# Performance work log

Hardware: AMD Instinct MI355X
Metric: run time of the kernel (lower is better)

The kernel has to match this reference:

```python
import jax, jax.numpy as jnp
import numpy as np

N = 100000   # nodes
E = 1600000  # edges (avg degree 16)
D = 128      # feature / hidden dim


def setup_inputs() -> dict:
    key = jax.random.key(0)
    k_x, k_e, k_w1, k_w2 = jax.random.split(key, 4)
    scale = 1.0 / np.sqrt(D)
    return {
        "x": jax.random.normal(k_x, (N, D), dtype=jnp.float32),
        "W1": jax.random.normal(k_w1, (D, D), dtype=jnp.float32) * scale,
        "b1": jnp.zeros((D,), dtype=jnp.float32),
        "W2": jax.random.normal(k_w2, (D, D), dtype=jnp.float32) * scale,
        "b2": jnp.zeros((D,), dtype=jnp.float32),
        "edge_index": jax.random.randint(k_e, (2, E), 0, N, dtype=jnp.int64),
    }


def _gcn_conv(h, src, dst, norm, W, b, n_nodes):
    # GCNConv: out = scatter_add(norm * (h @ W)[src] -> dst) + b
    y = h @ W                                   # [N, D] dense GEMM
    msgs = y[src] * norm[:, None]               # [E+N, D] gather + scale
    agg = jax.ops.segment_sum(msgs, dst, num_segments=n_nodes)  # scatter-add
    return agg + b


def reference(x, W1, b1, W2, b2, edge_index):
    n_nodes = x.shape[0]
    # add self loops (GCNConv default add_self_loops=True)
    loop = jnp.arange(n_nodes, dtype=edge_index.dtype)
    src = jnp.concatenate([edge_index[0], loop])
    dst = jnp.concatenate([edge_index[1], loop])
    # symmetric normalization: deg over destinations incl. self loops
    deg = jax.ops.segment_sum(jnp.ones_like(src, dtype=x.dtype), dst,
                              num_segments=n_nodes)
    dinv = jnp.where(deg > 0, jax.lax.rsqrt(deg), 0.0)
    norm = dinv[src] * dinv[dst]                # [E+N]
    # dropout in eval mode (identity); layer = conv -> ReLU, twice
    h = jax.nn.relu(_gcn_conv(x, src, dst, norm, W1, b1, n_nodes))
    h = jax.nn.relu(_gcn_conv(h, src, dst, norm, W2, b2, n_nodes))
    return h
```

## Files before the change

kernel.cpp:

```cpp
#include <hip/hip_runtime.h>
#include <hip/hip_bf16.h>


#define DIM 128
#define BSH 9
#define NBKT 196

typedef __attribute__((ext_vector_type(8))) short bf16x8;
typedef __attribute__((ext_vector_type(4))) float f32x4;

static __device__ __forceinline__ ushort bfbits(float f) {
    __hip_bfloat16 h = __float2bfloat16(f);
    return *(ushort*)&h;
}


__global__ __launch_bounds__(256) void k_bcount(const int* __restrict__ dst,
                                                int E, int* __restrict__ bcnt) {
    __shared__ int h[NBKT];
    int t = threadIdx.x;
    for (int b = t; b < NBKT; b += 256) h[b] = 0;
    __syncthreads();
    for (int e = blockIdx.x * 256 + t; e < E; e += gridDim.x * 256)
        atomicAdd(&h[dst[e] >> BSH], 1);
    __syncthreads();
    for (int b = t; b < NBKT; b += 256)
        if (h[b]) atomicAdd(&bcnt[b], h[b]);
}

__global__ void k_bscan(const int* __restrict__ bcnt, int* __restrict__ bbase,
                        int* __restrict__ bcur) {
    __shared__ int a[256], c[256];
    int t = threadIdx.x;
    int v = (t < NBKT) ? bcnt[t] : 0;
    a[t] = v;
    __syncthreads();
    int* A = a; int* B = c;
    for (int off = 1; off < 256; off <<= 1) {
        B[t] = A[t] + (t >= off ? A[t - off] : 0);
        __syncthreads();
        int* tmp = A; A = B; B = tmp;
    }
    int incl = A[t];
    if (t < NBKT) { int ex = incl - v; bbase[t] = ex; bcur[t] = ex; }
    if (t == NBKT - 1) bbase[NBKT] = incl;
}

__global__ __launch_bounds__(256) void k_bscatter(
    const int* __restrict__ src, const int* __restrict__ dst, int E,
    int* __restrict__ bcur, uint* __restrict__ out) {
    __shared__ uint stage[NBKT * 32];
    __shared__ int scnt[NBKT];
    __shared__ int needflush;
    int t = threadIdx.x;
    for (int b = t; b < NBKT; b += 256) scnt[b] = 0;
    if (t == 0) needflush = 0;
    __syncthreads();

    int per = (E + gridDim.x - 1) / gridDim.x;
    int s0 = blockIdx.x * per;
    int s1 = min(E, s0 + per);

    for (int base = s0; base < s1; base += 1024) {
#pragma unroll
        for (int k = 0; k < 4; ++k) {
            int e = base + t + k * 256;
            if (e < s1) {
                int d = dst[e];
                uint pr = ((uint)(d & 511) << 17) | (uint)src[e];
                int b = d >> BSH;
                int slot = atomicAdd(&scnt[b], 1);
                if (slot < 32) {
                    stage[b * 32 + slot] = pr;
                    if (slot == 31) needflush = 1;
                } else {
                    int c = atomicAdd(&bcur[b], 1);
                    out[c] = pr;
                }
            }
        }
        __syncthreads();
        if (needflush) {
            for (int bb = t; bb < NBKT; bb += 256) {
                if (scnt[bb] >= 32) {
                    int cur = atomicAdd(&bcur[bb], 32);
#pragma unroll
                    for (int k = 0; k < 32; ++k) out[cur + k] = stage[bb * 32 + k];
                    scnt[bb] = 0;
                }
            }
            __syncthreads();
            if (t == 0) needflush = 0;
            __syncthreads();
        }
    }
    for (int bb = t; bb < NBKT; bb += 256) {
        int c = scnt[bb]; if (c > 32) c = 32;
        if (c > 0) {
            int cur = atomicAdd(&bcur[bb], c);
            for (int k = 0; k < c; ++k) out[cur + k] = stage[bb * 32 + k];
        }
    }
}

__global__ __launch_bounds__(256) void k_bcsc(
    const uint* __restrict__ pairs, const int* __restrict__ bbase,
    int* __restrict__ rowptr, float* __restrict__ dinv,
    int* __restrict__ col, int n) {
    __shared__ int lh[512], ls[512];
    int b = blockIdx.x, t = threadIdx.x;
    int p0 = bbase[b], p1 = bbase[b + 1];
    int d0 = b << BSH;

    lh[t] = 0; lh[t + 256] = 0;
    __syncthreads();
    for (int i = p0 + t; i < p1; i += 256)
        atomicAdd(&lh[pairs[i] >> 17], 1);
    __syncthreads();

    int deg0 = lh[t], deg1 = lh[t + 256];
    int* A = lh; int* B = ls;
    for (int off = 1; off < 512; off <<= 1) {
        B[t]       = A[t]       + (t       >= off ? A[t - off]       : 0);
        B[t + 256] = A[t + 256] + (t + 256 >= off ? A[t + 256 - off] : 0);
        __syncthreads();
        int* tmp = A; A = B; B = tmp;
    }
    int ex0 = A[t] - deg0, ex1 = A[t + 256] - deg1;
    __syncthreads();
    B[t] = ex0; B[t + 256] = ex1;

    int nd = d0 + t;
    if (nd < n) { rowptr[nd] = p0 + ex0; dinv[nd] = rsqrtf((float)(deg0 + 1)); }
    nd = d0 + t + 256;
    if (nd < n) { rowptr[nd] = p0 + ex1; dinv[nd] = rsqrtf((float)(deg1 + 1)); }
    if (b == NBKT - 1 && t == 0) rowptr[n] = p1;
    __syncthreads();

    for (int i = p0 + t; i < p1; i += 256) {
        uint pr = pairs[i];
        int slot = p0 + atomicAdd(&B[pr >> 17], 1);
        col[slot] = (int)(pr & 0x1FFFFu);
    }
}

__global__ void k_split_w2(const float* __restrict__ W1,
                           const float* __restrict__ W2,
                           ushort* __restrict__ wpk1,
                           ushort* __restrict__ wpk2) {
    int g = blockIdx.x;
    const float* W   = (g < 64) ? W1 : W2;
    ushort* Wpk      = (g < 64) ? wpk1 : wpk2;
    int idx = (g & 63) * 256 + threadIdx.x;
    int j    = idx & 7;
    int lane = (idx >> 3) & 63;
    int ks   = (idx >> 9) & 3;
    int ct   = idx >> 11;
    int k  = ks * 32 + (lane >> 4) * 8 + j;
    int nn = ct * 16 + (lane & 15);
    float w = W[k * 128 + nn];
    __hip_bfloat16 hi = __float2bfloat16(w);
    float rem = w - __bfloat162float(hi);
    Wpk[idx]         = *(ushort*)&hi;
    Wpk[16384 + idx] = bfbits(rem);
}

template <int INF32>
__global__ __launch_bounds__(256, 2) void k_gemm_mfma(
    const void* __restrict__ xin, const ushort* __restrict__ Wpk,
    const float* __restrict__ dinv, ushort* __restrict__ y,
    int n, int ntiles) {
    __shared__ ushort Wl[32768];
    int t = threadIdx.x;
    {
        const uint4* s4 = (const uint4*)Wpk;
        uint4* d4 = (uint4*)Wl;
#pragma unroll
        for (int i = 0; i < 16; ++i) d4[t + 256 * i] = s4[t + 256 * i];
    }
    __syncthreads();

    const int wave = t >> 6, lane = t & 63;
    const int l15 = lane & 15, lg = lane >> 4;

    for (int tile = blockIdx.x; tile < ntiles; tile += gridDim.x) {
        int row0 = tile * 64 + wave * 16;
        int arow = row0 + l15;
        if (arow >= n) arow = n - 1;

        bf16x8 a[4];
        if (INF32) {
            const float* xp = (const float*)xin + (size_t)arow * 128 + lg * 8;
#pragma unroll
            for (int ks = 0; ks < 4; ++ks) {
                float4 f0 = *(const float4*)(xp + ks * 32);
                float4 f1 = *(const float4*)(xp + ks * 32 + 4);
                bf16x8 av;
                av[0] = (short)bfbits(f0.x); av[1] = (short)bfbits(f0.y);
                av[2] = (short)bfbits(f0.z); av[3] = (short)bfbits(f0.w);
                av[4] = (short)bfbits(f1.x); av[5] = (short)bfbits(f1.y);
                av[6] = (short)bfbits(f1.z); av[7] = (short)bfbits(f1.w);
                a[ks] = av;
            }
        } else {
            const ushort* xp = (const ushort*)xin + (size_t)arow * 128 + lg * 8;
#pragma unroll
            for (int ks = 0; ks < 4; ++ks)
                a[ks] = *(const bf16x8*)(xp + ks * 32);
        }

        f32x4 acc[8];
#pragma unroll
        for (int ct = 0; ct < 8; ++ct) acc[ct] = (f32x4)(0.f);

#pragma unroll
        for (int ks = 0; ks < 4; ++ks) {
#pragma unroll
            for (int ct = 0; ct < 8; ++ct) {
                bf16x8 b = *(const bf16x8*)&Wl[(size_t)((0 * 8 + ct) * 4 + ks) * 512 + lane * 8];
                acc[ct] = __builtin_amdgcn_mfma_f32_16x16x32_bf16(a[ks], b, acc[ct], 0, 0, 0);
            }
#pragma unroll
            for (int ct = 0; ct < 8; ++ct) {
                bf16x8 b = *(const bf16x8*)&Wl[(size_t)((1 * 8 + ct) * 4 + ks) * 512 + lane * 8];
                acc[ct] = __builtin_amdgcn_mfma_f32_16x16x32_bf16(a[ks], b, acc[ct], 0, 0, 0);
            }
        }

#pragma unroll
        for (int r = 0; r < 4; ++r) {
            int row = row0 + lg * 4 + r;
            if (row < n) {
                float dv = dinv[row];
                ushort* yr = y + (size_t)row * 128 + l15;
#pragma unroll
                for (int ct = 0; ct < 8; ++ct)
                    yr[ct * 16] = bfbits(acc[ct][r] * dv);
            }
        }
    }
}

template <int MODE>
__global__ __launch_bounds__(256) void k_agg2(
    const ushort* __restrict__ yb, const int* __restrict__ rowptr,
    const int* __restrict__ col, const float* __restrict__ dinv,
    const float* __restrict__ bias, void* __restrict__ outp, int n) {
    int t = threadIdx.x, lane = t & 63;
    int node = __builtin_amdgcn_readfirstlane(blockIdx.x * 4 + (t >> 6));
    if (node >= n) return;

    uint v0 = *(const uint*)(yb + (size_t)node * 128 + lane * 2);
    float ax = __uint_as_float(v0 << 16);
    float ay = __uint_as_float(v0 & 0xffff0000u);

    int lo = rowptr[node], hi = rowptr[node + 1];
    int i = lo;
    for (; i + 8 <= hi; i += 8) {
        uint w[8];
#pragma unroll
        for (int k = 0; k < 8; ++k)
            w[k] = *(const uint*)(yb + (size_t)col[i + k] * 128 + lane * 2);
#pragma unroll
        for (int k = 0; k < 8; ++k) {
            ax += __uint_as_float(w[k] << 16);
            ay += __uint_as_float(w[k] & 0xffff0000u);
        }
    }
    for (; i + 4 <= hi; i += 4) {
        uint w[4];
#pragma unroll
        for (int k = 0; k < 4; ++k)
            w[k] = *(const uint*)(yb + (size_t)col[i + k] * 128 + lane * 2);
#pragma unroll
        for (int k = 0; k < 4; ++k) {
            ax += __uint_as_float(w[k] << 16);
            ay += __uint_as_float(w[k] & 0xffff0000u);
        }
    }
    for (; i < hi; ++i) {
        uint w = *(const uint*)(yb + (size_t)col[i] * 128 + lane * 2);
        ax += __uint_as_float(w << 16);
        ay += __uint_as_float(w & 0xffff0000u);
    }

    float dv = dinv[node];
    float2 b = ((const float2*)bias)[lane];
    float ox = fmaxf(ax * dv + b.x, 0.f);
    float oy = fmaxf(ay * dv + b.y, 0.f);

    if (MODE == 0) {
        uint o = ((uint)bfbits(oy) << 16) | (uint)bfbits(ox);
        ((uint*)outp)[(size_t)node * 64 + lane] = o;
    } else {
        ((float2*)outp)[(size_t)node * 64 + lane] = make_float2(ox, oy);
    }
}


extern "C" void kernel_launch(void* const* d_in, const int* in_sizes, int n_in,
                              void* d_out, int out_size, void* d_ws, size_t ws_size,
                              hipStream_t stream) {
    const float* x  = (const float*)d_in[0];
    const float* W1 = (const float*)d_in[1];
    const float* b1 = (const float*)d_in[2];
    const float* W2 = (const float*)d_in[3];
    const float* b2 = (const float*)d_in[4];
    const int*   ei = (const int*)d_in[5];

    const int n = in_sizes[0] / DIM;
    const int E = in_sizes[5] / 2;
    const int* src = ei;
    const int* dst = ei + E;
    float* out = (float*)d_out;

    char* w = (char*)d_ws;
    ushort* y     = (ushort*)w;  w += (size_t)n * DIM * sizeof(ushort);
    ushort* h     = (ushort*)w;  w += (size_t)n * DIM * sizeof(ushort);
    uint*   bpair = (uint*)w;    w += (size_t)E * sizeof(uint);
    ushort* wpk1  = (ushort*)w;  w += 32768 * sizeof(ushort);
    ushort* wpk2  = (ushort*)w;  w += 32768 * sizeof(ushort);
    float*  dinv  = (float*)w;   w += (size_t)n * sizeof(float);
    int*    rowptr= (int*)w;     w += (size_t)(n + 4) * sizeof(int);
    int*    col   = (int*)w;     w += (size_t)E * sizeof(int);
    int*    bcnt  = (int*)w;     w += NBKT * sizeof(int);
    int*    bbase = (int*)w;     w += (NBKT + 4) * sizeof(int);
    int*    bcur  = (int*)w;     w += NBKT * sizeof(int);

    const int nbAgg  = (n + 3) / 4;
    const int ntiles = (n + 63) / 64;
    const int nbGemm = 512;

    hipMemsetAsync(bcnt, 0, NBKT * sizeof(int), stream);
    k_bcount  <<<256,  256, 0, stream>>>(dst, E, bcnt);
    k_bscan   <<<1,    256, 0, stream>>>(bcnt, bbase, bcur);
    k_bscatter<<<768,  256, 0, stream>>>(src, dst, E, bcur, bpair);
    k_bcsc    <<<NBKT, 256, 0, stream>>>(bpair, bbase, rowptr, dinv, col, n);

    k_split_w2<<<128, 256, 0, stream>>>(W1, W2, wpk1, wpk2);

    k_gemm_mfma<1><<<nbGemm, 256, 0, stream>>>(x, wpk1, dinv, y, n, ntiles);
    k_agg2<0><<<nbAgg, 256, 0, stream>>>(y, rowptr, col, dinv, b1, h, n);

    k_gemm_mfma<0><<<nbGemm, 256, 0, stream>>>(h, wpk2, dinv, y, n, ntiles);
    k_agg2<1><<<nbAgg, 256, 0, stream>>>(y, rowptr, col, dinv, b2, out, n);
}
```

Before: 371.0 us.

## Split aggregation across column slices with eight nodes per wave

Rewrites the neighbour aggregation so each block handles 32 nodes for one 16-column slice, with 8 lanes per node and 8 nodes per wave, instead of one full 128-wide row per wave. The aim is to keep more independent node gathers in flight and to spread work over more blocks, reducing the latency-bound serial loop per wave. The cost is smaller 32-byte gather segments per row, more rowptr/col reads because each slice re-reads the edge list, and divergence between nodes of different degree inside a wave. The 8-wide unroll is also dropped in favour of a 4-wide one.

```diff
diff --git a/kernel.cpp b/kernel.cpp
--- a/kernel.cpp
+++ b/kernel.cpp
@@ -242,58 +242,52 @@
 }
 
 template <int MODE>
-__global__ __launch_bounds__(256) void k_agg2(
+__global__ __launch_bounds__(256) void k_agg3(
     const ushort* __restrict__ yb, const int* __restrict__ rowptr,
     const int* __restrict__ col, const float* __restrict__ dinv,
     const float* __restrict__ bias, void* __restrict__ outp, int n) {
-    int t = threadIdx.x, lane = t & 63;
-    int node = __builtin_amdgcn_readfirstlane(blockIdx.x * 4 + (t >> 6));
+    int t = threadIdx.x;
+    int slice = blockIdx.x & 7;
+    int chunk = blockIdx.x >> 3;
+    int wave = t >> 6, lane = t & 63;
+    int node = chunk * 32 + wave * 8 + (lane >> 3);
     if (node >= n) return;
-
-    uint v0 = *(const uint*)(yb + (size_t)node * 128 + lane * 2);
+    int coff = slice * 16 + (lane & 7) * 2;
+
+    const ushort* base = yb + coff;
+    uint v0 = *(const uint*)(base + (size_t)node * 128);
     float ax = __uint_as_float(v0 << 16);
     float ay = __uint_as_float(v0 & 0xffff0000u);
 
     int lo = rowptr[node], hi = rowptr[node + 1];
     int i = lo;
-    for (; i + 8 <= hi; i += 8) {
-        uint w[8];
-#pragma unroll
-        for (int k = 0; k < 8; ++k)
-            w[k] = *(const uint*)(yb + (size_t)col[i + k] * 128 + lane * 2);
-#pragma unroll
-        for (int k = 0; k < 8; ++k) {
-            ax += __uint_as_float(w[k] << 16);
-            ay += __uint_as_float(w[k] & 0xffff0000u);
-        }
-    }
     for (; i + 4 <= hi; i += 4) {
-        uint w[4];
-#pragma unroll
-        for (int k = 0; k < 4; ++k)
-            w[k] = *(const uint*)(yb + (size_t)col[i + k] * 128 + lane * 2);
-#pragma unroll
-        for (int k = 0; k < 4; ++k) {
-            ax += __uint_as_float(w[k] << 16);
-            ay += __uint_as_float(w[k] & 0xffff0000u);
-        }
+        int s0 = col[i], s1 = col[i + 1], s2 = col[i + 2], s3 = col[i + 3];
+        uint w0 = *(const uint*)(base + (size_t)s0 * 128);
+        uint w1 = *(const uint*)(base + (size_t)s1 * 128);
+        uint w2 = *(const uint*)(base + (size_t)s2 * 128);
+        uint w3 = *(const uint*)(base + (size_t)s3 * 128);
+        ax += __uint_as_float(w0 << 16);  ay += __uint_as_float(w0 & 0xffff0000u);
+        ax += __uint_as_float(w1 << 16);  ay += __uint_as_float(w1 & 0xffff0000u);
+        ax += __uint_as_float(w2 << 16);  ay += __uint_as_float(w2 & 0xffff0000u);
+        ax += __uint_as_float(w3 << 16);  ay += __uint_as_float(w3 & 0xffff0000u);
     }
     for (; i < hi; ++i) {
-        uint w = *(const uint*)(yb + (size_t)col[i] * 128 + lane * 2);
+        uint w = *(const uint*)(base + (size_t)col[i] * 128);
         ax += __uint_as_float(w << 16);
         ay += __uint_as_float(w & 0xffff0000u);
     }
 
     float dv = dinv[node];
-    float2 b = ((const float2*)bias)[lane];
+    float2 b = ((const float2*)bias)[coff >> 1];
     float ox = fmaxf(ax * dv + b.x, 0.f);
     float oy = fmaxf(ay * dv + b.y, 0.f);
 
     if (MODE == 0) {
         uint o = ((uint)bfbits(oy) << 16) | (uint)bfbits(ox);
-        ((uint*)outp)[(size_t)node * 64 + lane] = o;
+        ((uint*)outp)[(size_t)node * 64 + (coff >> 1)] = o;
     } else {
-        ((float2*)outp)[(size_t)node * 64 + lane] = make_float2(ox, oy);
+        ((float2*)outp)[(size_t)node * 64 + (coff >> 1)] = make_float2(ox, oy);
     }
 }
 
@@ -327,7 +321,7 @@
     int*    bbase = (int*)w;     w += (NBKT + 4) * sizeof(int);
     int*    bcur  = (int*)w;     w += NBKT * sizeof(int);
 
-    const int nbAgg  = (n + 3) / 4;
+    const int nbAgg  = 8 * ((n + 31) / 32);
     const int ntiles = (n + 63) / 64;
     const int nbGemm = 512;
 
@@ -340,8 +334,8 @@
     k_split_w2<<<128, 256, 0, stream>>>(W1, W2, wpk1, wpk2);
 
     k_gemm_mfma<1><<<nbGemm, 256, 0, stream>>>(x, wpk1, dinv, y, n, ntiles);
-    k_agg2<0><<<nbAgg, 256, 0, stream>>>(y, rowptr, col, dinv, b1, h, n);
+    k_agg3<0><<<nbAgg, 256, 0, stream>>>(y, rowptr, col, dinv, b1, h, n);
 
     k_gemm_mfma<0><<<nbGemm, 256, 0, stream>>>(h, wpk2, dinv, y, n, ntiles);
-    k_agg2<1><<<nbAgg, 256, 0, stream>>>(y, rowptr, col, dinv, b2, out, n);
-}
+    k_agg3<1><<<nbAgg, 256, 0, stream>>>(y, rowptr, col, dinv, b2, out, n);
+}
```

Result: slower. 624.6 us (+68.4%).
